# Kernel optimization log

Measured on AMD Instinct MI355X. Metric: run time of the kernel, lower is better.

The kernel has to match this reference:

```python
import jax, jax.numpy as jnp
import numpy as np

EMBED = 1024
HEADS = 16
HEAD_DIM = EMBED // HEADS
EPS = 1e-5


def setup_inputs() -> dict:
    key = jax.random.key(0)
    ks = jax.random.split(key, 5)
    s = 1.0 / np.sqrt(EMBED)
    return {
        "x": jax.random.normal(ks[0], (2, 2048, EMBED), dtype=jnp.float32),
        "Wq": jax.random.normal(ks[1], (EMBED, EMBED), dtype=jnp.float32) * s,
        "Wk": jax.random.normal(ks[2], (EMBED, EMBED), dtype=jnp.float32) * s,
        "Wv": jax.random.normal(ks[3], (EMBED, EMBED), dtype=jnp.float32) * s,
        "Wout": jax.random.normal(ks[4], (EMBED, EMBED), dtype=jnp.float32) * s,
        "gamma": jnp.ones((EMBED,), dtype=jnp.float32),
        "beta": jnp.zeros((EMBED,), dtype=jnp.float32),
    }


def reference(x, Wq, Wk, Wv, Wout, gamma, beta):
    B, S, E = x.shape
    # nn.Linear(bias=False): y = x @ W.T; weight stored as [out, in]
    q = (x @ Wq.T).reshape(B, S, HEADS, HEAD_DIM)
    k = (x @ Wk.T).reshape(B, S, HEADS, HEAD_DIM)
    v = (x @ Wv.T).reshape(B, S, HEADS, HEAD_DIM)
    scale = 1.0 / jnp.sqrt(jnp.float32(HEAD_DIM)).astype(x.dtype)
    scores = jnp.einsum("bqhd,bkhd->bhqk", q, k) * scale  # [B,H,S,S]
    probs = jax.nn.softmax(scores, axis=-1)
    attn = jnp.einsum("bhqk,bkhd->bqhd", probs, v).reshape(B, S, E)
    out = attn @ Wout.T
    y = out + x
    mu = jnp.mean(y, axis=-1, keepdims=True)
    var = jnp.var(y, axis=-1, keepdims=True)
    return (y - mu) * jax.lax.rsqrt(var + EPS) * gamma + beta
```

## Files before the change

### kernel.cpp

```cpp
#include <hip/hip_runtime.h>
#include <hip/hip_bf16.h>
#include <cstdint>
#include <cstddef>

#define SEQ   2048
#define BATCH 2
#define NROWS 4096
#define EMB   1024
#define NHEAD 16
#define HD    64
#define KVBLK 64
#define NT    (SEQ / KVBLK)

typedef __attribute__((ext_vector_type(8))) short bf16x8;
typedef __attribute__((ext_vector_type(4))) float f32x4;
typedef __attribute__((ext_vector_type(16))) float f32x16;
typedef __attribute__((ext_vector_type(2))) int i32x2;
typedef __hip_bfloat16 bf16_t;

__device__ __forceinline__ int swz(int row, int cb) { return cb ^ ((row & 7) << 4); }

__device__ __forceinline__ void plswap(int a, int b, int& ra, int& rb) {
#if __has_builtin(__builtin_amdgcn_permlane32_swap)
  i32x2 r = __builtin_amdgcn_permlane32_swap(a, b, false, false);
  ra = r[0]; rb = r[1];
#else
  const int pa = __shfl_xor(a, 32), pb = __shfl_xor(b, 32);
  const bool lo = (threadIdx.x & 63) < 32;
  ra = lo ? a : pb;
  rb = lo ? pa : b;
#endif
}
__device__ __forceinline__ float pairmax32(float v) {
  int r0, r1;
  plswap(__float_as_int(v), __float_as_int(v), r0, r1);
  return fmaxf(__int_as_float(r0), __int_as_float(r1));
}
__device__ __forceinline__ float pairsum32(float v) {
  int r0, r1;
  plswap(__float_as_int(v), __float_as_int(v), r0, r1);
  return __int_as_float(r0) + __int_as_float(r1);
}

__global__ __launch_bounds__(256) void cast_f32_to_bf16(const float* __restrict__ in,
                                                        bf16_t* __restrict__ out, int n4) {
  int i = blockIdx.x * 256 + threadIdx.x;
  if (i >= n4) return;
  float4 v = reinterpret_cast<const float4*>(in)[i];
  union { ushort4 u; bf16_t h[4]; } o;
  o.h[0] = __float2bfloat16(v.x);
  o.h[1] = __float2bfloat16(v.y);
  o.h[2] = __float2bfloat16(v.z);
  o.h[3] = __float2bfloat16(v.w);
  reinterpret_cast<ushort4*>(out)[i] = o.u;
}

__global__ __launch_bounds__(256) void cast4_w(const float* __restrict__ a,
                                               const float* __restrict__ b,
                                               const float* __restrict__ c,
                                               const float* __restrict__ d,
                                               bf16_t* __restrict__ oa, bf16_t* __restrict__ ob,
                                               bf16_t* __restrict__ oc, bf16_t* __restrict__ od,
                                               int n4) {
  const int z = blockIdx.z;
  const float* in = (z == 0) ? a : (z == 1) ? b : (z == 2) ? c : d;
  bf16_t* out = (z == 0) ? oa : (z == 1) ? ob : (z == 2) ? oc : od;
  int i = blockIdx.x * 256 + threadIdx.x;
  if (i >= n4) return;
  float4 v = reinterpret_cast<const float4*>(in)[i];
  union { ushort4 u; bf16_t h[4]; } o;
  o.h[0] = __float2bfloat16(v.x);
  o.h[1] = __float2bfloat16(v.y);
  o.h[2] = __float2bfloat16(v.z);
  o.h[3] = __float2bfloat16(v.w);
  reinterpret_cast<ushort4*>(out)[i] = o.u;
}

template <int MODE>
__device__ __forceinline__ void gemm128_body(const bf16_t* __restrict__ A,
                                             const bf16_t* __restrict__ W,
                                             bf16_t* __restrict__ Ob,
                                             float* __restrict__ Of,
                                             const float* __restrict__ Res) {
  __shared__ __align__(16) bf16_t As[128 * 32];
  __shared__ __align__(16) bf16_t Bs[128 * 32];
  const int tid = threadIdx.x;
  const int lane = tid & 63;
  const int wv = tid >> 6;
  const int wm = wv >> 1, wn = wv & 1;
  const int brow = blockIdx.y * 128;
  const int bcol = blockIdx.x * 128;
  const int lr = lane & 15, lg = lane >> 4;

  f32x4 acc[4][4] = {};

  auto* As3 = (__attribute__((address_space(3))) char*)As;
  auto* Bs3 = (__attribute__((address_space(3))) char*)Bs;

  for (int k0 = 0; k0 < EMB; k0 += 32) {
    __syncthreads();
#pragma unroll
    for (int i = 0; i < 2; ++i) {
      const int chunk = i * 256 + tid;
      const int row = chunk >> 2;
      const int kc = (chunk & 3) * 8;
      const bf16_t* ga = A + (size_t)(brow + row) * EMB + k0 + kc;
      const bf16_t* gb = W + (size_t)(bcol + row) * EMB + k0 + kc;
      __builtin_amdgcn_global_load_lds((const __attribute__((address_space(1))) void*)ga,
                                       (__attribute__((address_space(3))) void*)(As3 + chunk * 16),
                                       16, 0, 0);
      __builtin_amdgcn_global_load_lds((const __attribute__((address_space(1))) void*)gb,
                                       (__attribute__((address_space(3))) void*)(Bs3 + chunk * 16),
                                       16, 0, 0);
    }
    __syncthreads();

    bf16x8 af[4], bfr[4];
#pragma unroll
    for (int m = 0; m < 4; ++m)
      af[m] = *reinterpret_cast<const bf16x8*>(&As[(wm * 64 + m * 16 + lr) * 32 + lg * 8]);
#pragma unroll
    for (int n = 0; n < 4; ++n)
      bfr[n] = *reinterpret_cast<const bf16x8*>(&Bs[(wn * 64 + n * 16 + lr) * 32 + lg * 8]);
#pragma unroll
    for (int m = 0; m < 4; ++m)
#pragma unroll
      for (int n = 0; n < 4; ++n)
        acc[m][n] = __builtin_amdgcn_mfma_f32_16x16x32_bf16(af[m], bfr[n], acc[m][n], 0, 0, 0);
  }

  const int r0 = brow + wm * 64;
  const int c0 = bcol + wn * 64;
#pragma unroll
  for (int m = 0; m < 4; ++m)
#pragma unroll
    for (int n = 0; n < 4; ++n) {
      if (MODE == 2) {
        const int row0 = r0 + m * 16 + lg * 4;
        const int col = c0 + n * 16 + lr;
        const size_t vt_row = (size_t)(row0 >> 11) * 1024 + col;
        const int s = row0 & 2047;
        union { uint2 u2; bf16_t h[4]; } pu;
#pragma unroll
        for (int r = 0; r < 4; ++r) pu.h[r] = __float2bfloat16(acc[m][n][r]);
        *reinterpret_cast<uint2*>(Ob + vt_row * SEQ + s) = pu.u2;
      } else {
#pragma unroll
        for (int r = 0; r < 4; ++r) {
          const int row = r0 + m * 16 + lg * 4 + r;
          const int col = c0 + n * 16 + lr;
          const size_t idx = (size_t)row * EMB + col;
          if (MODE == 0) Ob[idx] = __float2bfloat16(acc[m][n][r]);
          else Of[idx] = acc[m][n][r] + Res[idx];
        }
      }
    }
}

__global__ __launch_bounds__(256) void gemm_qkv(const bf16_t* __restrict__ X,
                                                const bf16_t* __restrict__ Wq,
                                                const bf16_t* __restrict__ Wk,
                                                const bf16_t* __restrict__ Wv,
                                                bf16_t* __restrict__ Q,
                                                bf16_t* __restrict__ K,
                                                bf16_t* __restrict__ Vt) {
  if (blockIdx.z == 0)      gemm128_body<0>(X, Wq, Q, nullptr, nullptr);
  else if (blockIdx.z == 1) gemm128_body<0>(X, Wk, K, nullptr, nullptr);
  else                      gemm128_body<2>(X, Wv, Vt, nullptr, nullptr);
}

__global__ __launch_bounds__(256) void gemm_out(const bf16_t* __restrict__ Attn,
                                                const bf16_t* __restrict__ Wo,
                                                float* __restrict__ Y,
                                                const float* __restrict__ X) {
  gemm128_body<1>(Attn, Wo, nullptr, Y, X);
}

__global__ __launch_bounds__(256) void attn_kernel(const bf16_t* __restrict__ Q,
                                                   const bf16_t* __restrict__ K,
                                                   const bf16_t* __restrict__ Vt,
                                                   bf16_t* __restrict__ Oout) {
  __shared__ __align__(16) bf16_t Ks[3][KVBLK * 64];
  __shared__ __align__(16) bf16_t Vs[3][KVBLK * 64];

  const int tid = threadIdx.x;
  const int lane = tid & 63;
  const int wv = tid >> 6;
  const int lq = lane & 31;
  const int lh = lane >> 5;

  const int f = blockIdx.x + 16 * blockIdx.y + 256 * blockIdx.z;
  const int w = (f & 7) * 64 + (f >> 3);
  const int qb = w & 15;
  const int h = (w >> 4) & 15;
  const int b = w >> 8;

  const size_t baseRow = (size_t)b * SEQ;
  const int hoff = h * HD;
  const int q0 = qb * 128 + wv * 32;

  const float qscale = 0.125f * 1.44269504f;
  bf16x8 qf[4];
#pragma unroll
  for (int ks = 0; ks < 4; ++ks) {
    bf16x8 t = *reinterpret_cast<const bf16x8*>(
        &Q[(baseRow + q0 + lq) * EMB + hoff + ks * 16 + lh * 8]);
    union { bf16x8 v; bf16_t h[8]; } u;
    u.v = t;
#pragma unroll
    for (int e = 0; e < 8; ++e)
      u.h[e] = __float2bfloat16(__bfloat162float(u.h[e]) * qscale);
    qf[ks] = u.v;
  }

  f32x16 o0 = {}, o1 = {};
  float mrow = -1e30f, lrow = 0.f;

  auto* Ks3 = (__attribute__((address_space(3))) char*)&Ks[0][0];
  auto* Vs3 = (__attribute__((address_space(3))) char*)&Vs[0][0];

  const int srow = tid >> 3;
  const int scb = swz(srow, (tid & 7) * 16) >> 1;
  const bf16_t* kp = K + (baseRow + srow) * EMB + hoff + scb;
  const bf16_t* vp = Vt + ((size_t)(b * 1024 + hoff) + srow) * SEQ + scb;

  auto stage = [&](int buf) {
#pragma unroll
    for (int i = 0; i < 2; ++i) {
      const int c = i * 256 + tid;
      __builtin_amdgcn_global_load_lds(
          (const __attribute__((address_space(1))) void*)(kp + i * 32 * EMB),
          (__attribute__((address_space(3))) void*)(Ks3 + buf * 8192 + c * 16), 16, 0, 0);
      __builtin_amdgcn_global_load_lds(
          (const __attribute__((address_space(1))) void*)(vp + i * 32 * SEQ),
          (__attribute__((address_space(3))) void*)(Vs3 + buf * 8192 + c * 16), 16, 0, 0);
    }
    kp += KVBLK * EMB;
    vp += KVBLK;
  };

  auto QKT = [&](int buf, f32x16& s0, f32x16& s1) {
    const char* Kb = (const char*)Ks + buf * 8192;
    s0 = (f32x16){};
    s1 = (f32x16){};
    __builtin_amdgcn_s_setprio(1);
#pragma unroll
    for (int ks = 0; ks < 4; ++ks) {
      bf16x8 kf0 = *reinterpret_cast<const bf16x8*>(Kb + lq * 128 + swz(lq, ks * 32 + lh * 16));
      s0 = __builtin_amdgcn_mfma_f32_32x32x16_bf16(kf0, qf[ks], s0, 0, 0, 0);
    }
#pragma unroll
    for (int ks = 0; ks < 4; ++ks) {
      bf16x8 kf1 = *reinterpret_cast<const bf16x8*>(Kb + (32 + lq) * 128 + swz(lq, ks * 32 + lh * 16));
      s1 = __builtin_amdgcn_mfma_f32_32x32x16_bf16(kf1, qf[ks], s1, 0, 0, 0);
    }
    __builtin_amdgcn_s_setprio(0);
  };

  auto FIN = [&](f32x16& st0, f32x16& st1, int buf) {
    const char* Vb = (const char*)Vs + buf * 8192;
    float mx = -1e30f;
#pragma unroll
    for (int r = 0; r < 16; ++r) mx = fmaxf(mx, st0[r]);
#pragma unroll
    for (int r = 0; r < 16; ++r) mx = fmaxf(mx, st1[r]);
    mx = pairmax32(mx);

    if (!__all(mx - mrow <= 8.f)) {
      const float mnew = fmaxf(mrow, mx);
      const float al = __builtin_amdgcn_exp2f(mrow - mnew);
      mrow = mnew;
      lrow *= al;
#pragma unroll
      for (int r = 0; r < 16; ++r) o0[r] *= al;
#pragma unroll
      for (int r = 0; r < 16; ++r) o1[r] *= al;
    }

#pragma unroll
    for (int r = 0; r < 16; ++r) st0[r] = __builtin_amdgcn_exp2f(st0[r] - mrow);
#pragma unroll
    for (int r = 0; r < 16; ++r) st1[r] = __builtin_amdgcn_exp2f(st1[r] - mrow);
    {
      float a0 = (st0[0] + st0[1]) + (st0[2] + st0[3]);
      float a1 = (st0[4] + st0[5]) + (st0[6] + st0[7]);
      float a2 = (st0[8] + st0[9]) + (st0[10] + st0[11]);
      float a3 = (st0[12] + st0[13]) + (st0[14] + st0[15]);
      float b0 = (st1[0] + st1[1]) + (st1[2] + st1[3]);
      float b1 = (st1[4] + st1[5]) + (st1[6] + st1[7]);
      float b2 = (st1[8] + st1[9]) + (st1[10] + st1[11]);
      float b3 = (st1[12] + st1[13]) + (st1[14] + st1[15]);
      lrow += pairsum32(((a0 + a1) + (a2 + a3)) + ((b0 + b1) + (b2 + b3)));
    }

    bf16x8 pb[4];
#pragma unroll
    for (int jh = 0; jh < 2; ++jh)
#pragma unroll
      for (int sub = 0; sub < 2; ++sub) {
        const f32x16& s = jh ? st1 : st0;
        int w01, w23, w45, w67;
        asm("v_cvt_pk_bf16_f32 %0, %1, %2" : "=v"(w01) : "v"(s[sub * 8 + 0]), "v"(s[sub * 8 + 1]));
        asm("v_cvt_pk_bf16_f32 %0, %1, %2" : "=v"(w23) : "v"(s[sub * 8 + 2]), "v"(s[sub * 8 + 3]));
        asm("v_cvt_pk_bf16_f32 %0, %1, %2" : "=v"(w45) : "v"(s[sub * 8 + 4]), "v"(s[sub * 8 + 5]));
        asm("v_cvt_pk_bf16_f32 %0, %1, %2" : "=v"(w67) : "v"(s[sub * 8 + 6]), "v"(s[sub * 8 + 7]));
        int d0, d1, d2, d3;
        plswap(w01, w45, d0, d2);
        plswap(w23, w67, d1, d3);
        union { int i[4]; bf16x8 v; } u;
        u.i[0] = d0; u.i[1] = d1; u.i[2] = d2; u.i[3] = d3;
        pb[jh * 2 + sub] = u.v;
      }

    __builtin_amdgcn_s_setprio(1);
#pragma unroll
    for (int js = 0; js < 4; ++js) {
      bf16x8 vf0 = *reinterpret_cast<const bf16x8*>(Vb + lq * 128 + swz(lq, js * 32 + lh * 16));
      o0 = __builtin_amdgcn_mfma_f32_32x32x16_bf16(vf0, pb[js], o0, 0, 0, 0);
    }
#pragma unroll
    for (int js = 0; js < 4; ++js) {
      bf16x8 vf1 = *reinterpret_cast<const bf16x8*>(Vb + (32 + lq) * 128 + swz(lq, js * 32 + lh * 16));
      o1 = __builtin_amdgcn_mfma_f32_32x32x16_bf16(vf1, pb[js], o1, 0, 0, 0);
    }
    __builtin_amdgcn_s_setprio(0);
  };

  f32x16 sA0, sA1, sB0, sB1;

  stage(0);
  __syncthreads();
  stage(1);
  QKT(0, sA0, sA1);

  for (int t = 1; t + 1 < NT; t += 2) {
    __syncthreads();
    stage((t + 1) % 3);
    QKT(t % 3, sB0, sB1);
    FIN(sA0, sA1, (t - 1) % 3);
    __syncthreads();
    if (t + 2 < NT) stage((t + 2) % 3);
    QKT((t + 1) % 3, sA0, sA1);
    FIN(sB0, sB1, t % 3);
  }
  __syncthreads();
  QKT((NT - 1) % 3, sB0, sB1);
  FIN(sA0, sA1, (NT - 2) % 3);
  FIN(sB0, sB1, (NT - 1) % 3);

  const float inv = 1.f / lrow;
  const size_t orow = (baseRow + q0 + lq) * EMB + hoff;
#pragma unroll
  for (int g = 0; g < 4; ++g) {
    union { uint2 u2; bf16_t h[4]; } pu;
#pragma unroll
    for (int r = 0; r < 4; ++r) pu.h[r] = __float2bfloat16(o0[g * 4 + r] * inv);
    *reinterpret_cast<uint2*>(Oout + orow + g * 8 + lh * 4) = pu.u2;
  }
#pragma unroll
  for (int g = 0; g < 4; ++g) {
    union { uint2 u2; bf16_t h[4]; } pu;
#pragma unroll
    for (int r = 0; r < 4; ++r) pu.h[r] = __float2bfloat16(o1[g * 4 + r] * inv);
    *reinterpret_cast<uint2*>(Oout + orow + 32 + g * 8 + lh * 4) = pu.u2;
  }
}

__global__ __launch_bounds__(256) void ln_kernel(const float* __restrict__ Y,
                                                 const float* __restrict__ gamma,
                                                 const float* __restrict__ beta,
                                                 float* __restrict__ Out) {
  const int row = blockIdx.x;
  const int tid = threadIdx.x;
  const float4 v = reinterpret_cast<const float4*>(Y + (size_t)row * EMB)[tid];
  float s = v.x + v.y + v.z + v.w;
  float s2 = v.x * v.x + v.y * v.y + v.z * v.z + v.w * v.w;
#pragma unroll
  for (int m = 1; m < 64; m <<= 1) {
    s += __shfl_xor(s, m);
    s2 += __shfl_xor(s2, m);
  }
  __shared__ float ws[4], ws2[4];
  const int w = tid >> 6;
  if ((tid & 63) == 0) { ws[w] = s; ws2[w] = s2; }
  __syncthreads();
  s = ws[0] + ws[1] + ws[2] + ws[3];
  s2 = ws2[0] + ws2[1] + ws2[2] + ws2[3];
  const float mu = s * (1.f / EMB);
  const float var = s2 * (1.f / EMB) - mu * mu;
  const float rstd = rsqrtf(var + 1e-5f);
  const float4 g = reinterpret_cast<const float4*>(gamma)[tid];
  const float4 bt = reinterpret_cast<const float4*>(beta)[tid];
  float4 ov;
  ov.x = (v.x - mu) * rstd * g.x + bt.x;
  ov.y = (v.y - mu) * rstd * g.y + bt.y;
  ov.z = (v.z - mu) * rstd * g.z + bt.z;
  ov.w = (v.w - mu) * rstd * g.w + bt.w;
  reinterpret_cast<float4*>(Out + (size_t)row * EMB)[tid] = ov;
}

extern "C" void kernel_launch(void* const* d_in, const int* in_sizes, int n_in,
                              void* d_out, int out_size, void* d_ws, size_t ws_size,
                              hipStream_t stream) {
  const float* x = (const float*)d_in[0];
  const float* Wq = (const float*)d_in[1];
  const float* Wk = (const float*)d_in[2];
  const float* Wv = (const float*)d_in[3];
  const float* Wo = (const float*)d_in[4];
  const float* gamma = (const float*)d_in[5];
  const float* beta = (const float*)d_in[6];
  float* out = (float*)d_out;

  char* p = (char*)d_ws;
  const size_t sz_rows_bf = (size_t)NROWS * EMB * sizeof(bf16_t);
  const size_t sz_w_bf = (size_t)EMB * EMB * sizeof(bf16_t);
  bf16_t* xb = (bf16_t*)p; p += sz_rows_bf;
  bf16_t* wqb = (bf16_t*)p; p += sz_w_bf;
  bf16_t* wkb = (bf16_t*)p; p += sz_w_bf;
  bf16_t* wvb = (bf16_t*)p; p += sz_w_bf;
  bf16_t* wob = (bf16_t*)p; p += sz_w_bf;
  bf16_t* q = (bf16_t*)p; p += sz_rows_bf;
  bf16_t* k = (bf16_t*)p; p += sz_rows_bf;
  bf16_t* vt = (bf16_t*)p; p += sz_rows_bf;
  bf16_t* attn = (bf16_t*)p; p += sz_rows_bf;
  float* y = (float*)q;

  const int n4x = NROWS * EMB / 4;
  const int n4w = EMB * EMB / 4;
  cast_f32_to_bf16<<<n4x / 256, 256, 0, stream>>>(x, xb, n4x);
  cast4_w<<<dim3(n4w / 256, 1, 4), 256, 0, stream>>>(Wq, Wk, Wv, Wo, wqb, wkb, wvb, wob, n4w);

  gemm_qkv<<<dim3(EMB / 128, NROWS / 128, 3), 256, 0, stream>>>(xb, wqb, wkb, wvb, q, k, vt);

  attn_kernel<<<dim3(SEQ / 128, NHEAD, BATCH), 256, 0, stream>>>(q, k, vt, attn);

  gemm_out<<<dim3(EMB / 128, NROWS / 128, 1), 256, 0, stream>>>(attn, wob, y, x);

  ln_kernel<<<NROWS, 256, 0, stream>>>(y, gamma, beta, out);
}
```

Baseline: 128.8 us.

## Split attention KV range in two and merge partials in a combine kernel

Attention blocks now each process half of the key/value sequence, doubling the grid from 512 to 1024 blocks so more compute units are busy on the 256-CU device. Each half writes a normalized bf16 partial output plus its running max and sum, and a new combine kernel rescales and merges the two halves into the attention buffer. This adds an extra launch, extra global traffic for the partials, and an extra bf16 rounding step. It falls back to the old path if the workspace is too small.

```diff
diff --git a/kernel.cpp b/kernel.cpp
--- a/kernel.cpp
+++ b/kernel.cpp
@@ -10,7 +10,7 @@
 #define NHEAD 16
 #define HD    64
 #define KVBLK 64
-#define NT    (SEQ / KVBLK)
+#define NQROWS (BATCH * NHEAD * SEQ)
 
 typedef __attribute__((ext_vector_type(8))) short bf16x8;
 typedef __attribute__((ext_vector_type(4))) float f32x4;
@@ -176,10 +176,13 @@
   gemm128_body<1>(Attn, Wo, nullptr, Y, X);
 }
 
+template <bool SPLIT>
 __global__ __launch_bounds__(256) void attn_kernel(const bf16_t* __restrict__ Q,
                                                    const bf16_t* __restrict__ K,
                                                    const bf16_t* __restrict__ Vt,
-                                                   bf16_t* __restrict__ Oout) {
+                                                   bf16_t* __restrict__ Oout,
+                                                   bf16_t* __restrict__ Opart,
+                                                   float2* __restrict__ Ml) {
   __shared__ __align__(16) bf16_t Ks[3][KVBLK * 64];
   __shared__ __align__(16) bf16_t Vs[3][KVBLK * 64];
 
@@ -189,11 +192,25 @@
   const int lq = lane & 31;
   const int lh = lane >> 5;
 
-  const int f = blockIdx.x + 16 * blockIdx.y + 256 * blockIdx.z;
-  const int w = (f & 7) * 64 + (f >> 3);
-  const int qb = w & 15;
-  const int h = (w >> 4) & 15;
-  const int b = w >> 8;
+  int qb, h, b, split;
+  if (SPLIT) {
+    const int f = blockIdx.x + 16 * blockIdx.y + 256 * blockIdx.z;
+    const int w = (f & 7) * 128 + (f >> 3);
+    qb = w & 15;
+    h = (w >> 4) & 15;
+    const int bs = w >> 8;
+    b = bs >> 1;
+    split = bs & 1;
+  } else {
+    const int f = blockIdx.x + 16 * blockIdx.y + 256 * blockIdx.z;
+    const int w = (f & 7) * 64 + (f >> 3);
+    qb = w & 15;
+    h = (w >> 4) & 15;
+    b = w >> 8;
+    split = 0;
+  }
+  const int NT = SPLIT ? (SEQ / (2 * KVBLK)) : (SEQ / KVBLK);
+  const int j0base = split * (SEQ / 2);
 
   const size_t baseRow = (size_t)b * SEQ;
   const int hoff = h * HD;
@@ -221,8 +238,8 @@
 
   const int srow = tid >> 3;
   const int scb = swz(srow, (tid & 7) * 16) >> 1;
-  const bf16_t* kp = K + (baseRow + srow) * EMB + hoff + scb;
-  const bf16_t* vp = Vt + ((size_t)(b * 1024 + hoff) + srow) * SEQ + scb;
+  const bf16_t* kp = K + (baseRow + j0base + srow) * EMB + hoff + scb;
+  const bf16_t* vp = Vt + ((size_t)(b * 1024 + hoff) + srow) * SEQ + j0base + scb;
 
   auto stage = [&](int buf) {
 #pragma unroll
@@ -349,20 +366,70 @@
   FIN(sB0, sB1, (NT - 1) % 3);
 
   const float inv = 1.f / lrow;
-  const size_t orow = (baseRow + q0 + lq) * EMB + hoff;
-#pragma unroll
-  for (int g = 0; g < 4; ++g) {
-    union { uint2 u2; bf16_t h[4]; } pu;
-#pragma unroll
-    for (int r = 0; r < 4; ++r) pu.h[r] = __float2bfloat16(o0[g * 4 + r] * inv);
-    *reinterpret_cast<uint2*>(Oout + orow + g * 8 + lh * 4) = pu.u2;
-  }
-#pragma unroll
-  for (int g = 0; g < 4; ++g) {
-    union { uint2 u2; bf16_t h[4]; } pu;
-#pragma unroll
-    for (int r = 0; r < 4; ++r) pu.h[r] = __float2bfloat16(o1[g * 4 + r] * inv);
-    *reinterpret_cast<uint2*>(Oout + orow + 32 + g * 8 + lh * 4) = pu.u2;
+  if (SPLIT) {
+    const size_t gidx = ((size_t)(b * NHEAD + h)) * SEQ + q0 + lq;
+    bf16_t* pdst = Opart + ((size_t)split * NQROWS + gidx) * HD;
+#pragma unroll
+    for (int g = 0; g < 4; ++g) {
+      union { uint2 u2; bf16_t h[4]; } pu;
+#pragma unroll
+      for (int r = 0; r < 4; ++r) pu.h[r] = __float2bfloat16(o0[g * 4 + r] * inv);
+      *reinterpret_cast<uint2*>(pdst + g * 8 + lh * 4) = pu.u2;
+    }
+#pragma unroll
+    for (int g = 0; g < 4; ++g) {
+      union { uint2 u2; bf16_t h[4]; } pu;
+#pragma unroll
+      for (int r = 0; r < 4; ++r) pu.h[r] = __float2bfloat16(o1[g * 4 + r] * inv);
+      *reinterpret_cast<uint2*>(pdst + 32 + g * 8 + lh * 4) = pu.u2;
+    }
+    if (lh == 0) Ml[(size_t)split * NQROWS + gidx] = make_float2(mrow, lrow);
+  } else {
+    const size_t orow = (baseRow + q0 + lq) * EMB + hoff;
+#pragma unroll
+    for (int g = 0; g < 4; ++g) {
+      union { uint2 u2; bf16_t h[4]; } pu;
+#pragma unroll
+      for (int r = 0; r < 4; ++r) pu.h[r] = __float2bfloat16(o0[g * 4 + r] * inv);
+      *reinterpret_cast<uint2*>(Oout + orow + g * 8 + lh * 4) = pu.u2;
+    }
+#pragma unroll
+    for (int g = 0; g < 4; ++g) {
+      union { uint2 u2; bf16_t h[4]; } pu;
+#pragma unroll
+      for (int r = 0; r < 4; ++r) pu.h[r] = __float2bfloat16(o1[g * 4 + r] * inv);
+      *reinterpret_cast<uint2*>(Oout + orow + 32 + g * 8 + lh * 4) = pu.u2;
+    }
+  }
+}
+
+__global__ __launch_bounds__(256) void attn_combine(const bf16_t* __restrict__ Opart,
+                                                    const float2* __restrict__ Ml,
+                                                    bf16_t* __restrict__ Oout) {
+  const size_t gidx = (size_t)blockIdx.x * 256 + threadIdx.x;
+  const float2 ml0 = Ml[gidx];
+  const float2 ml1 = Ml[NQROWS + gidx];
+  const float mmax = fmaxf(ml0.x, ml1.x);
+  const float a0 = __builtin_amdgcn_exp2f(ml0.x - mmax) * ml0.y;
+  const float a1 = __builtin_amdgcn_exp2f(ml1.x - mmax) * ml1.y;
+  const float inv = 1.f / (a0 + a1);
+  const float w0 = a0 * inv, w1 = a1 * inv;
+
+  const int s = (int)(gidx & (SEQ - 1));
+  const int h = (int)((gidx >> 11) & (NHEAD - 1));
+  const int b = (int)(gidx >> 15);
+  bf16_t* dst = Oout + ((size_t)(b * SEQ + s)) * EMB + h * HD;
+  const bf16x8* p0 = reinterpret_cast<const bf16x8*>(Opart + gidx * HD);
+  const bf16x8* p1 = reinterpret_cast<const bf16x8*>(Opart + ((size_t)NQROWS + gidx) * HD);
+#pragma unroll
+  for (int c = 0; c < 8; ++c) {
+    union { bf16x8 v; bf16_t h[8]; } u0, u1, uo;
+    u0.v = p0[c];
+    u1.v = p1[c];
+#pragma unroll
+    for (int e = 0; e < 8; ++e)
+      uo.h[e] = __float2bfloat16(w0 * __bfloat162float(u0.h[e]) + w1 * __bfloat162float(u1.h[e]));
+    reinterpret_cast<bf16x8*>(dst)[c] = uo.v;
   }
 }
 
@@ -425,6 +492,10 @@
   bf16_t* attn = (bf16_t*)p; p += sz_rows_bf;
   float* y = (float*)q;
 
+  bf16_t* opart = (bf16_t*)p; p += (size_t)2 * NQROWS * HD * sizeof(bf16_t);
+  float2* ml = (float2*)p; p += (size_t)2 * NQROWS * sizeof(float2);
+  const bool use_split = ((size_t)(p - (char*)d_ws) <= ws_size);
+
   const int n4x = NROWS * EMB / 4;
   const int n4w = EMB * EMB / 4;
   cast_f32_to_bf16<<<n4x / 256, 256, 0, stream>>>(x, xb, n4x);
@@ -432,7 +503,12 @@
 
   gemm_qkv<<<dim3(EMB / 128, NROWS / 128, 3), 256, 0, stream>>>(xb, wqb, wkb, wvb, q, k, vt);
 
-  attn_kernel<<<dim3(SEQ / 128, NHEAD, BATCH), 256, 0, stream>>>(q, k, vt, attn);
+  if (use_split) {
+    attn_kernel<true><<<dim3(16, 16, 2 * BATCH), 256, 0, stream>>>(q, k, vt, attn, opart, ml);
+    attn_combine<<<NQROWS / 256, 256, 0, stream>>>(opart, ml, attn);
+  } else {
+    attn_kernel<false><<<dim3(16, 16, BATCH), 256, 0, stream>>>(q, k, vt, attn, nullptr, nullptr);
+  }
 
   gemm_out<<<dim3(EMB / 128, NROWS / 128, 1), 256, 0, stream>>>(attn, wob, y, x);
 
```

After: 140.7 us. 9.3% more time.

## Split attention KV range across two wave groups and merge partial softmax in LDS

Applied to the files above, without the earlier changes.

The attention block grows to 512 threads. Two groups of four waves each process half of the KV sequence for the same 128 queries, and their partial max, sum and output are merged through LDS at the end. This doubles the waves per block to raise occupancy and latency hiding, since the grid is only 512 blocks. The software pipeline drops from a three-buffer interleaved QK/PV schedule to a simpler double buffer with a barrier every iteration. That may lose intra-wave overlap and adds a 64KB LDS footprint plus merge overhead.

```diff
diff --git a/kernel.cpp b/kernel.cpp
--- a/kernel.cpp
+++ b/kernel.cpp
@@ -10,7 +10,7 @@
 #define NHEAD 16
 #define HD    64
 #define KVBLK 64
-#define NT    (SEQ / KVBLK)
+#define NTG   16
 
 typedef __attribute__((ext_vector_type(8))) short bf16x8;
 typedef __attribute__((ext_vector_type(4))) float f32x4;
@@ -176,28 +176,29 @@
   gemm128_body<1>(Attn, Wo, nullptr, Y, X);
 }
 
-__global__ __launch_bounds__(256) void attn_kernel(const bf16_t* __restrict__ Q,
-                                                   const bf16_t* __restrict__ K,
-                                                   const bf16_t* __restrict__ Vt,
-                                                   bf16_t* __restrict__ Oout) {
-  __shared__ __align__(16) bf16_t Ks[3][KVBLK * 64];
-  __shared__ __align__(16) bf16_t Vs[3][KVBLK * 64];
+__global__ __launch_bounds__(512, 4) void attn_kernel(const bf16_t* __restrict__ Q,
+                                                      const bf16_t* __restrict__ K,
+                                                      const bf16_t* __restrict__ Vt,
+                                                      bf16_t* __restrict__ Oout) {
+  __shared__ __align__(16) char L[65536];
 
   const int tid = threadIdx.x;
   const int lane = tid & 63;
   const int wv = tid >> 6;
+  const int w = wv & 3;
+  const int sg = wv >> 2;
   const int lq = lane & 31;
   const int lh = lane >> 5;
 
   const int f = blockIdx.x + 16 * blockIdx.y + 256 * blockIdx.z;
-  const int w = (f & 7) * 64 + (f >> 3);
-  const int qb = w & 15;
-  const int h = (w >> 4) & 15;
-  const int b = w >> 8;
+  const int ww = (f & 7) * 64 + (f >> 3);
+  const int qb = ww & 15;
+  const int h = (ww >> 4) & 15;
+  const int b = ww >> 8;
 
   const size_t baseRow = (size_t)b * SEQ;
   const int hoff = h * HD;
-  const int q0 = qb * 128 + wv * 32;
+  const int q0 = qb * 128 + w * 32;
 
   const float qscale = 0.125f * 1.44269504f;
   bf16x8 qf[4];
@@ -216,49 +217,54 @@
   f32x16 o0 = {}, o1 = {};
   float mrow = -1e30f, lrow = 0.f;
 
-  auto* Ks3 = (__attribute__((address_space(3))) char*)&Ks[0][0];
-  auto* Vs3 = (__attribute__((address_space(3))) char*)&Vs[0][0];
-
-  const int srow = tid >> 3;
-  const int scb = swz(srow, (tid & 7) * 16) >> 1;
-  const bf16_t* kp = K + (baseRow + srow) * EMB + hoff + scb;
-  const bf16_t* vp = Vt + ((size_t)(b * 1024 + hoff) + srow) * SEQ + scb;
+  auto* L3 = (__attribute__((address_space(3))) char*)L;
+  const int gbase = sg * 32768;
+
+  const int stid = tid & 255;
+  const int srow = stid >> 3;
+  const int scb = swz(srow, (stid & 7) * 16) >> 1;
+  const bf16_t* kp = K + (baseRow + sg * 1024 + srow) * EMB + hoff + scb;
+  const bf16_t* vp = Vt + ((size_t)(b * 1024 + hoff) + srow) * SEQ + sg * 1024 + scb;
 
   auto stage = [&](int buf) {
 #pragma unroll
     for (int i = 0; i < 2; ++i) {
-      const int c = i * 256 + tid;
+      const int c = i * 256 + stid;
       __builtin_amdgcn_global_load_lds(
           (const __attribute__((address_space(1))) void*)(kp + i * 32 * EMB),
-          (__attribute__((address_space(3))) void*)(Ks3 + buf * 8192 + c * 16), 16, 0, 0);
+          (__attribute__((address_space(3))) void*)(L3 + gbase + buf * 8192 + c * 16), 16, 0, 0);
       __builtin_amdgcn_global_load_lds(
           (const __attribute__((address_space(1))) void*)(vp + i * 32 * SEQ),
-          (__attribute__((address_space(3))) void*)(Vs3 + buf * 8192 + c * 16), 16, 0, 0);
+          (__attribute__((address_space(3))) void*)(L3 + gbase + 16384 + buf * 8192 + c * 16), 16, 0, 0);
     }
     kp += KVBLK * EMB;
     vp += KVBLK;
   };
 
-  auto QKT = [&](int buf, f32x16& s0, f32x16& s1) {
-    const char* Kb = (const char*)Ks + buf * 8192;
-    s0 = (f32x16){};
-    s1 = (f32x16){};
+  stage(0);
+  __syncthreads();
+
+  for (int t = 0; t < NTG; ++t) {
+    const int cur = t & 1;
+    if (t + 1 < NTG) stage(cur ^ 1);
+
+    const char* Kb = (const char*)L + gbase + cur * 8192;
+    const char* Vb = (const char*)L + gbase + 16384 + cur * 8192;
+
+    f32x16 st0 = {}, st1 = {};
     __builtin_amdgcn_s_setprio(1);
 #pragma unroll
     for (int ks = 0; ks < 4; ++ks) {
       bf16x8 kf0 = *reinterpret_cast<const bf16x8*>(Kb + lq * 128 + swz(lq, ks * 32 + lh * 16));
-      s0 = __builtin_amdgcn_mfma_f32_32x32x16_bf16(kf0, qf[ks], s0, 0, 0, 0);
+      st0 = __builtin_amdgcn_mfma_f32_32x32x16_bf16(kf0, qf[ks], st0, 0, 0, 0);
     }
 #pragma unroll
     for (int ks = 0; ks < 4; ++ks) {
       bf16x8 kf1 = *reinterpret_cast<const bf16x8*>(Kb + (32 + lq) * 128 + swz(lq, ks * 32 + lh * 16));
-      s1 = __builtin_amdgcn_mfma_f32_32x32x16_bf16(kf1, qf[ks], s1, 0, 0, 0);
+      st1 = __builtin_amdgcn_mfma_f32_32x32x16_bf16(kf1, qf[ks], st1, 0, 0, 0);
     }
     __builtin_amdgcn_s_setprio(0);
-  };
-
-  auto FIN = [&](f32x16& st0, f32x16& st1, int buf) {
-    const char* Vb = (const char*)Vs + buf * 8192;
+
     float mx = -1e30f;
 #pragma unroll
     for (int r = 0; r < 16; ++r) mx = fmaxf(mx, st0[r]);
@@ -324,45 +330,44 @@
       o1 = __builtin_amdgcn_mfma_f32_32x32x16_bf16(vf1, pb[js], o1, 0, 0, 0);
     }
     __builtin_amdgcn_s_setprio(0);
-  };
-
-  f32x16 sA0, sA1, sB0, sB1;
-
-  stage(0);
+
+    __syncthreads();
+  }
+
+  float* OL = reinterpret_cast<float*>(L + 32768);
+  float2* MLx = reinterpret_cast<float2*>(L);
   __syncthreads();
-  stage(1);
-  QKT(0, sA0, sA1);
-
-  for (int t = 1; t + 1 < NT; t += 2) {
-    __syncthreads();
-    stage((t + 1) % 3);
-    QKT(t % 3, sB0, sB1);
-    FIN(sA0, sA1, (t - 1) % 3);
-    __syncthreads();
-    if (t + 2 < NT) stage((t + 2) % 3);
-    QKT((t + 1) % 3, sA0, sA1);
-    FIN(sB0, sB1, t % 3);
+  if (sg == 1) {
+    MLx[w * 64 + lane] = make_float2(mrow, lrow);
+#pragma unroll
+    for (int r = 0; r < 16; ++r) OL[w * 2048 + r * 64 + lane] = o0[r];
+#pragma unroll
+    for (int r = 0; r < 16; ++r) OL[w * 2048 + (16 + r) * 64 + lane] = o1[r];
   }
   __syncthreads();
-  QKT((NT - 1) % 3, sB0, sB1);
-  FIN(sA0, sA1, (NT - 2) % 3);
-  FIN(sB0, sB1, (NT - 1) % 3);
-
-  const float inv = 1.f / lrow;
-  const size_t orow = (baseRow + q0 + lq) * EMB + hoff;
-#pragma unroll
-  for (int g = 0; g < 4; ++g) {
-    union { uint2 u2; bf16_t h[4]; } pu;
-#pragma unroll
-    for (int r = 0; r < 4; ++r) pu.h[r] = __float2bfloat16(o0[g * 4 + r] * inv);
-    *reinterpret_cast<uint2*>(Oout + orow + g * 8 + lh * 4) = pu.u2;
-  }
-#pragma unroll
-  for (int g = 0; g < 4; ++g) {
-    union { uint2 u2; bf16_t h[4]; } pu;
-#pragma unroll
-    for (int r = 0; r < 4; ++r) pu.h[r] = __float2bfloat16(o1[g * 4 + r] * inv);
-    *reinterpret_cast<uint2*>(Oout + orow + 32 + g * 8 + lh * 4) = pu.u2;
+  if (sg == 0) {
+    const float2 ml1 = MLx[w * 64 + lane];
+    const float M = fmaxf(mrow, ml1.x);
+    const float f0 = __builtin_amdgcn_exp2f(mrow - M);
+    const float f1 = __builtin_amdgcn_exp2f(ml1.x - M);
+    const float inv = 1.f / (f0 * lrow + f1 * ml1.y);
+    const size_t orow = (baseRow + q0 + lq) * EMB + hoff;
+#pragma unroll
+    for (int g = 0; g < 4; ++g) {
+      union { uint2 u2; bf16_t h[4]; } pu;
+#pragma unroll
+      for (int r = 0; r < 4; ++r)
+        pu.h[r] = __float2bfloat16((f0 * o0[g * 4 + r] + f1 * OL[w * 2048 + (g * 4 + r) * 64 + lane]) * inv);
+      *reinterpret_cast<uint2*>(Oout + orow + g * 8 + lh * 4) = pu.u2;
+    }
+#pragma unroll
+    for (int g = 0; g < 4; ++g) {
+      union { uint2 u2; bf16_t h[4]; } pu;
+#pragma unroll
+      for (int r = 0; r < 4; ++r)
+        pu.h[r] = __float2bfloat16((f0 * o1[g * 4 + r] + f1 * OL[w * 2048 + (16 + g * 4 + r) * 64 + lane]) * inv);
+      *reinterpret_cast<uint2*>(Oout + orow + 32 + g * 8 + lh * 4) = pu.u2;
+    }
   }
 }
 
@@ -432,7 +437,7 @@
 
   gemm_qkv<<<dim3(EMB / 128, NROWS / 128, 3), 256, 0, stream>>>(xb, wqb, wkb, wvb, q, k, vt);
 
-  attn_kernel<<<dim3(SEQ / 128, NHEAD, BATCH), 256, 0, stream>>>(q, k, vt, attn);
+  attn_kernel<<<dim3(16, 16, BATCH), 512, 0, stream>>>(q, k, vt, attn);
 
   gemm_out<<<dim3(EMB / 128, NROWS / 128, 1), 256, 0, stream>>>(attn, wob, y, x);
 
```

Result: faster. 123.3 us (-4.3%).
